# Kernel tuning notes

Hardware: AMD Instinct MI355X
Metric: run time of the kernel (lower is better)

## Reference

```python
import jax, jax.numpy as jnp
import numpy as np
import math

EMBED_DIM = 512
NUM_HEADS = 8
NUM_LAYERS = 6
NUM_CLASSES = 8
MAX_POS = 100
LN_EPS = 1e-5


def setup_inputs() -> dict:
    key = jax.random.key(0)
    ks = jax.random.split(key, 12)
    D, H, L, C = EMBED_DIM, NUM_HEADS, NUM_LAYERS, NUM_CLASSES
    B, M = 64, 20
    s = 0.02
    def p(k, shape):
        return jax.random.normal(k, shape, jnp.float32) * s
    return {
        "context_tokens": jax.random.normal(ks[0], (B, M, D), jnp.float32),
        "pos_enc": jax.random.normal(ks[1], (1, MAX_POS, D), jnp.float32),
        "sa_w": p(ks[2], (L, 3 * D, D)), "sa_b": jnp.zeros((L, 3 * D), jnp.float32),
        "sa_ow": p(ks[3], (L, D, D)), "sa_ob": jnp.zeros((L, D), jnp.float32),
        "ca_w": p(ks[4], (L, 3 * D, D)), "ca_b": jnp.zeros((L, 3 * D), jnp.float32),
        "ca_ow": p(ks[5], (L, D, D)), "ca_ob": jnp.zeros((L, D), jnp.float32),
        "ln1_g": jnp.ones((L, D), jnp.float32), "ln1_b": jnp.zeros((L, D), jnp.float32),
        "ln2_g": jnp.ones((L, D), jnp.float32), "ln2_b": jnp.zeros((L, D), jnp.float32),
        "ln3_g": jnp.ones((L, D), jnp.float32), "ln3_b": jnp.zeros((L, D), jnp.float32),
        "ffn_w1": p(ks[6], (L, 4 * D, D)), "ffn_b1": jnp.zeros((L, 4 * D), jnp.float32),
        "ffn_w2": p(ks[7], (L, D, 4 * D)), "ffn_b2": jnp.zeros((L, D), jnp.float32),
        "out_w": p(ks[8], (C, D)), "out_b": jnp.zeros((C,), jnp.float32),
        "max_tokens": 30,
    }


def _ln(x, g, b):
    m = jnp.mean(x, axis=-1, keepdims=True)
    v = jnp.mean(jnp.square(x - m), axis=-1, keepdims=True)
    return (x - m) * jax.lax.rsqrt(v + LN_EPS) * g + b


def _mha(q_in, kv_in, w, b, ow, ob, causal):
    # w: (3D, D) packed q/k/v projections (PyTorch in_proj), ow: (D, D)
    D = q_in.shape[-1]
    H = NUM_HEADS
    hd = D // H
    qw, kw, vw = w[:D], w[D:2 * D], w[2 * D:]
    bq, bk, bv = b[:D], b[D:2 * D], b[2 * D:]
    q = q_in @ qw.T + bq
    k = kv_in @ kw.T + bk
    v = kv_in @ vw.T + bv
    B, Sq = q.shape[0], q.shape[1]
    Sk = k.shape[1]
    q = q.reshape(B, Sq, H, hd)
    k = k.reshape(B, Sk, H, hd)
    v = v.reshape(B, Sk, H, hd)
    scores = jnp.einsum('bqhd,bkhd->bhqk', q, k) * (1.0 / math.sqrt(hd))
    if causal:
        mask = jnp.tril(jnp.ones((Sq, Sk), dtype=bool))
        scores = jnp.where(mask, scores, -jnp.inf)
    attn = jax.nn.softmax(scores, axis=-1)
    out = jnp.einsum('bhqk,bkhd->bqhd', attn, v).reshape(B, Sq, D)
    return out @ ow.T + ob


def _forward(context_tokens, pos_enc, sa_w, sa_b, sa_ow, sa_ob, ca_w, ca_b,
             ca_ow, ca_ob, ln1_g, ln1_b, ln2_g, ln2_b, ln3_g, ln3_b,
             ffn_w1, ffn_b1, ffn_w2, ffn_b2, out_w, out_b, max_tokens):
    gen = context_tokens  # (B, M, D), grows each step (full recompute, no KV cache)
    outs = []
    for t in range(max_tokens):
        S = gen.shape[1]
        x = gen + pos_enc[:, :S, :]
        for i in range(NUM_LAYERS):
            # norm_first pre-LN GPT-2 style TransformerDecoderLayer
            x = x + _mha(_ln(x, ln1_g[i], ln1_b[i]), _ln(x, ln1_g[i], ln1_b[i]),
                         sa_w[i], sa_b[i], sa_ow[i], sa_ob[i], causal=True)
            x = x + _mha(_ln(x, ln2_g[i], ln2_b[i]), context_tokens,
                         ca_w[i], ca_b[i], ca_ow[i], ca_ob[i], causal=False)
            h = _ln(x, ln3_g[i], ln3_b[i])
            h = jax.nn.gelu(h @ ffn_w1[i].T + ffn_b1[i], approximate=False)
            x = x + (h @ ffn_w2[i].T + ffn_b2[i])
        last = x[:, -1:, :]
        outs.append(last @ out_w.T + out_b)
        gen = jnp.concatenate([gen, last], axis=1)
    return jnp.concatenate(outs, axis=1)  # (B, max_tokens, num_classes)


def reference(context_tokens, pos_enc, sa_w, sa_b, sa_ow, sa_ob, ca_w, ca_b,
              ca_ow, ca_ob, ln1_g, ln1_b, ln2_g, ln2_b, ln3_g, ln3_b,
              ffn_w1, ffn_b1, ffn_w2, ffn_b2, out_w, out_b, max_tokens):
    return _forward(context_tokens, pos_enc, sa_w, sa_b, sa_ow, sa_ob, ca_w, ca_b,
                    ca_ow, ca_ob, ln1_g, ln1_b, ln2_g, ln2_b, ln3_g, ln3_b,
                    ffn_w1, ffn_b1, ffn_w2, ffn_b2, out_w, out_b, max_tokens)
```

## Files before the change

kernel.cpp:

```cpp
#include <hip/hip_runtime.h>
#include <math.h>

#define F4(p) (*reinterpret_cast<const float4*>(p))

constexpr int D    = 512;
constexpr int H    = 8;
constexpr int HD   = 64;
constexpr int NL   = 6;
constexpr int NB   = 64;
constexpr int M    = 20;
constexpr int T    = 30;
constexpr int SMAX = 49;
constexpr int NR   = NB * M;
constexpr float EPS   = 1e-5f;
constexpr float SCALE = 0.125f;

#define GM_PLAIN 0
#define GM_QKV   1

__device__ __forceinline__ float gelu_f(float x){
  return 0.5f * x * (1.f + erff(x * 0.70710678118654752f));
}

template<int K>
__device__ __forceinline__ float dot8(const float* __restrict__ w, const float* x, int j){
  float a0 = 0.f, a1 = 0.f;
  #pragma unroll
  for (int r = 0; r < K/64; r++){
    int d = j*4 + r*64;
    float4 w0 = F4(w + d);        float4 w1 = F4(w + d + 32);
    float4 x0 = F4(x + d);        float4 x1 = F4(x + d + 32);
    a0 += w0.x*x0.x + w0.y*x0.y + w0.z*x0.z + w0.w*x0.w;
    a1 += w1.x*x1.x + w1.y*x1.y + w1.z*x1.z + w1.w*x1.w;
  }
  float a = a0 + a1;
  a += __shfl_xor(a, 4, 8);
  a += __shfl_xor(a, 2, 8);
  a += __shfl_xor(a, 1, 8);
  return a;
}

__device__ __forceinline__ float dot16_2048(const float* __restrict__ w, const float* x, int j){
  float a0 = 0.f, a1 = 0.f;
  #pragma unroll
  for (int r = 0; r < 16; r++){
    int d = j*4 + r*128;
    float4 w0 = F4(w + d);        float4 w1 = F4(w + d + 64);
    float4 x0 = F4(x + d);        float4 x1 = F4(x + d + 64);
    a0 += w0.x*x0.x + w0.y*x0.y + w0.z*x0.z + w0.w*x0.w;
    a1 += w1.x*x1.x + w1.y*x1.y + w1.z*x1.z + w1.w*x1.w;
  }
  float a = a0 + a1;
  a += __shfl_xor(a, 8, 16);
  a += __shfl_xor(a, 4, 16);
  a += __shfl_xor(a, 2, 16);
  a += __shfl_xor(a, 1, 16);
  return a;
}


__device__ __forceinline__ float wave_sum64(float v){
  #pragma unroll
  for (int o = 32; o > 0; o >>= 1) v += __shfl_down(v, o, 64);
  return v;
}

__device__ __forceinline__ float block_sum256(float v, float* red){
  v = wave_sum64(v);
  int wid = threadIdx.x >> 6, lane = threadIdx.x & 63;
  if (lane == 0) red[wid] = v;
  __syncthreads();
  if (threadIdx.x == 0) red[0] = red[0] + red[1] + red[2] + red[3];
  __syncthreads();
  float tot = red[0];
  __syncthreads();
  return tot;
}

__global__ __launch_bounds__(256) void k_embed(const float* __restrict__ ctx,
    const float* __restrict__ pos, float* __restrict__ X0){
  int r = blockIdx.x, t = threadIdx.x, s = r % M;
  X0[(size_t)r*D + t]       = ctx[(size_t)r*D + t]       + pos[(size_t)s*D + t];
  X0[(size_t)r*D + t + 256] = ctx[(size_t)r*D + t + 256] + pos[(size_t)s*D + t + 256];
}

__global__ __launch_bounds__(256) void k_ln(const float* __restrict__ x, float* __restrict__ y,
    const float* __restrict__ g, const float* __restrict__ bb){
  __shared__ float red[4];
  int r = blockIdx.x, t = threadIdx.x;
  const float* xr = x + (size_t)r*D;
  float v0 = xr[t], v1 = xr[t+256];
  float mean = block_sum256(v0+v1, red) * (1.f/D);
  float d0 = v0-mean, d1 = v1-mean;
  float var = block_sum256(d0*d0 + d1*d1, red) * (1.f/D);
  float rs = rsqrtf(var + EPS);
  float* yr = y + (size_t)r*D;
  yr[t]     = d0*rs*g[t]     + bb[t];
  yr[t+256] = d1*rs*g[t+256] + bb[t+256];
}

__global__ __launch_bounds__(256) void k_gemm(
    const float* __restrict__ A, const float* __restrict__ W,
    const float* __restrict__ bias, const float* __restrict__ res,
    float* __restrict__ C, int K, int ldc, int gelu_flag,
    float* __restrict__ q0, float* __restrict__ kc, float* __restrict__ vc, int mode){
  __shared__ __align__(16) float As[32][64];
  __shared__ __align__(16) float Ws[32][64];
  int m0 = blockIdx.x*64, n0 = blockIdx.y*64;
  int t = threadIdx.x, tx = t & 15, ty = t >> 4;
  float acc[4][4] = {};
  for (int k0 = 0; k0 < K; k0 += 32){
    #pragma unroll
    for (int i = 0; i < 2; i++){
      int idx = t + i*256;
      int m = idx & 63, k4 = idx >> 6;
      float4 a = F4(A + (size_t)(m0+m)*K + k0 + k4*4);
      As[k4*4+0][m]=a.x; As[k4*4+1][m]=a.y; As[k4*4+2][m]=a.z; As[k4*4+3][m]=a.w;
      float4 w = F4(W + (size_t)(n0+m)*K + k0 + k4*4);
      Ws[k4*4+0][m]=w.x; Ws[k4*4+1][m]=w.y; Ws[k4*4+2][m]=w.z; Ws[k4*4+3][m]=w.w;
    }
    __syncthreads();
    #pragma unroll
    for (int k = 0; k < 32; k++){
      float4 a = *reinterpret_cast<float4*>(&As[k][ty*4]);
      float4 w = *reinterpret_cast<float4*>(&Ws[k][tx*4]);
      float av[4] = {a.x,a.y,a.z,a.w};
      float wv[4] = {w.x,w.y,w.z,w.w};
      #pragma unroll
      for (int i = 0; i < 4; i++)
        #pragma unroll
        for (int jj = 0; jj < 4; jj++) acc[i][jj] += av[i]*wv[jj];
    }
    __syncthreads();
  }
  #pragma unroll
  for (int i = 0; i < 4; i++){
    int row = m0 + ty*4 + i;
    #pragma unroll
    for (int jj = 0; jj < 4; jj++){
      int col = n0 + tx*4 + jj;
      float v = acc[i][jj] + bias[col];
      if (res) v += res[(size_t)row*ldc + col];
      if (gelu_flag) v = gelu_f(v);
      if (mode == GM_PLAIN){
        C[(size_t)row*ldc + col] = v;
      } else {
        if (col < D) q0[(size_t)row*D + col] = v;
        else {
          int b = row / M, s = row % M;
          float* dst = (col < 2*D) ? kc : vc;
          dst[((size_t)b*SMAX + s)*D + (col & (D-1))] = v;
        }
      }
    }
  }
}

__global__ __launch_bounds__(256) void k_sattn_pre(const float* __restrict__ Q0,
    const float* __restrict__ kc, const float* __restrict__ vc, float* __restrict__ AT0){
  int b = blockIdx.x >> 3, h = blockIdx.x & 7, t = threadIdx.x;
  __shared__ __align__(16) float q[M][HD], kk[M][HD], vv[M][HD];
  __shared__ float sc[M][M];
  for (int idx = t; idx < M*HD; idx += 256){
    int s = idx >> 6, e = idx & 63;
    q[s][e]  = Q0[((size_t)b*M + s)*D + h*HD + e];
    kk[s][e] = kc[((size_t)b*SMAX + s)*D + h*HD + e];
    vv[s][e] = vc[((size_t)b*SMAX + s)*D + h*HD + e];
  }
  __syncthreads();
  for (int idx = t; idx < M*M; idx += 256){
    int qs = idx / M, ks = idx % M;
    if (ks <= qs){
      float s = 0.f;
      #pragma unroll
      for (int e = 0; e < HD; e++) s += q[qs][e]*kk[ks][e];
      sc[qs][ks] = s * SCALE;
    }
  }
  __syncthreads();
  if (t < M){
    float mx = -1e30f;
    for (int ks = 0; ks <= t; ks++) mx = fmaxf(mx, sc[t][ks]);
    float sum = 0.f;
    for (int ks = 0; ks <= t; ks++){ float e = expf(sc[t][ks]-mx); sc[t][ks] = e; sum += e; }
    float inv = 1.f/sum;
    for (int ks = 0; ks <= t; ks++) sc[t][ks] *= inv;
  }
  __syncthreads();
  for (int idx = t; idx < M*HD; idx += 256){
    int qs = idx >> 6, e = idx & 63;
    float o = 0.f;
    for (int ks = 0; ks <= qs; ks++) o += sc[qs][ks]*vv[ks][e];
    AT0[((size_t)b*M + qs)*D + h*HD + e] = o;
  }
}

__global__ __launch_bounds__(256) void k_cattn_pre(const float* __restrict__ Q0,
    const float* __restrict__ ckv, float* __restrict__ AT0){
  int b = blockIdx.x >> 3, h = blockIdx.x & 7, t = threadIdx.x;
  __shared__ __align__(16) float q[M][HD], kk[M][HD], vv[M][HD];
  __shared__ float sc[M][M];
  for (int idx = t; idx < M*HD; idx += 256){
    int s = idx >> 6, e = idx & 63;
    q[s][e]  = Q0[((size_t)b*M + s)*D + h*HD + e];
    kk[s][e] = ckv[((size_t)b*M + s)*1024 + h*HD + e];
    vv[s][e] = ckv[((size_t)b*M + s)*1024 + D + h*HD + e];
  }
  __syncthreads();
  for (int idx = t; idx < M*M; idx += 256){
    int qs = idx / M, ks = idx % M;
    float s = 0.f;
    #pragma unroll
    for (int e = 0; e < HD; e++) s += q[qs][e]*kk[ks][e];
    sc[qs][ks] = s * SCALE;
  }
  __syncthreads();
  if (t < M){
    float mx = -1e30f;
    for (int ks = 0; ks < M; ks++) mx = fmaxf(mx, sc[t][ks]);
    float sum = 0.f;
    for (int ks = 0; ks < M; ks++){ float e = expf(sc[t][ks]-mx); sc[t][ks] = e; sum += e; }
    float inv = 1.f/sum;
    for (int ks = 0; ks < M; ks++) sc[t][ks] *= inv;
  }
  __syncthreads();
  for (int idx = t; idx < M*HD; idx += 256){
    int qs = idx >> 6, e = idx & 63;
    float o = 0.f;
    for (int ks = 0; ks < M; ks++) o += sc[qs][ks]*vv[ks][e];
    AT0[((size_t)b*M + qs)*D + h*HD + e] = o;
  }
}


__device__ __forceinline__ float bsum1024(float v, float* red, int t){
  #pragma unroll
  for (int o = 32; o > 0; o >>= 1) v += __shfl_xor(v, o, 64);
  if ((t & 63) == 0) red[t >> 6] = v;
  __syncthreads();
  if (t == 0){
    float s = 0.f;
    #pragma unroll
    for (int i = 0; i < 16; i++) s += red[i];
    red[16] = s;
  }
  __syncthreads();
  return red[16];
}

__device__ __forceinline__ void ln_ip(const float* xx, float* yy,
    const float* __restrict__ g, const float* __restrict__ bb, float* red, int t){
  float v = (t < D) ? xx[t] : 0.f;
  float mean = bsum1024(v, red, t) * (1.f/D);
  float dd = (t < D) ? (v - mean) : 0.f;
  float var = bsum1024(dd*dd, red, t) * (1.f/D);
  float rs = rsqrtf(var + EPS);
  if (t < D) yy[t] = dd*rs*g[t] + bb[t];
}

__device__ __forceinline__ void logits_pos(float* x, const float* __restrict__ outw,
    const float* __restrict__ outb, const float* __restrict__ pos,
    float* __restrict__ out, int b, int t, int st, int pn){
  if (t < D){
    int c = t >> 6, lane = t & 63;
    const float* wr = outw + (size_t)c*D + lane*8;
    const float* xr = x + lane*8;
    float4 w0 = F4(wr), w1 = F4(wr + 4);
    float4 x0 = F4(xr), x1 = F4(xr + 4);
    float a = w0.x*x0.x + w0.y*x0.y + w0.z*x0.z + w0.w*x0.w
            + w1.x*x1.x + w1.y*x1.y + w1.z*x1.z + w1.w*x1.w;
    #pragma unroll
    for (int o = 32; o > 0; o >>= 1) a += __shfl_xor(a, o, 64);
    if (lane == 0) out[((size_t)b*T + st)*8 + c] = a + outb[c];
  }
  __syncthreads();
  if (t < D) x[t] += pos[(size_t)pn*D + t];
  __syncthreads();
}

__global__ __launch_bounds__(1024) void k_chain(
    const float* __restrict__ X0, const float* __restrict__ pos,
    const float* __restrict__ sa_w, const float* __restrict__ sa_b,
    const float* __restrict__ sa_ow, const float* __restrict__ sa_ob,
    const float* __restrict__ ca_w, const float* __restrict__ ca_b,
    const float* __restrict__ ca_ow, const float* __restrict__ ca_ob,
    const float* __restrict__ ln1g, const float* __restrict__ ln1b,
    const float* __restrict__ ln2g, const float* __restrict__ ln2b,
    const float* __restrict__ ln3g, const float* __restrict__ ln3b,
    const float* __restrict__ fw1, const float* __restrict__ fb1,
    const float* __restrict__ fw2, const float* __restrict__ fb2,
    const float* __restrict__ outw, const float* __restrict__ outb,
    float* __restrict__ kcache, float* __restrict__ vcache,
    const float* __restrict__ ckv, float* __restrict__ out)
{
  const int b = blockIdx.x, t = threadIdx.x;
  const int j8 = t & 7, j16 = t & 15;
  __shared__ __align__(16) float x[D], xn[D], q[D], at[D], kcur[D], vcur[D];
  __shared__ __align__(16) float hh[2048];
  __shared__ float sc[H][SMAX + 7];
  __shared__ float red[17];

  if (t < D) x[t] = X0[((size_t)b*M + (M-1))*D + t];
  __syncthreads();

  logits_pos(x, outw, outb, pos, out, b, t, 0, M);

  for (int st = 1; st < T; st++){
    const int p = M - 1 + st, S = p + 1;
    for (int l = 0; l < NL; l++){
      float* kb = kcache + ((size_t)l*NB + b)*SMAX*D;
      float* vb = vcache + ((size_t)l*NB + b)*SMAX*D;
      const float* cb_ = ckv + ((size_t)l*NB + b)*M*1024;

      ln_ip(x, xn, ln1g + l*D, ln1b + l*D, red, t);
      __syncthreads();

      {
        const float* w = sa_w + (size_t)l*3*D*D;
        const float* bias = sa_b + (size_t)l*3*D;
        for (int pass = 0; pass < 12; pass++){
          int o = pass*128 + (t >> 3);
          float r = dot8<512>(w + (size_t)o*D, xn, j8);
          if (j8 == 0){
            r += bias[o];
            if (o < D) q[o] = r;
            else if (o < 2*D){ kcur[o-D] = r; kb[(size_t)p*D + (o-D)] = r; }
            else { vcur[o-2*D] = r; vb[(size_t)p*D + (o-2*D)] = r; }
          }
        }
      }
      __syncthreads();

      {
        int h = t >> 7, kslot = (t & 127) >> 3;
        const float* qh = q + h*HD;
        float4 x0 = F4(qh + j8*4), x1 = F4(qh + j8*4 + 32);
        for (int ks = kslot; ks < S; ks += 16){
          const float* kr = (ks == p) ? (kcur + h*HD) : (kb + (size_t)ks*D + h*HD);
          float4 w0 = F4(kr + j8*4), w1 = F4(kr + j8*4 + 32);
          float a = w0.x*x0.x + w0.y*x0.y + w0.z*x0.z + w0.w*x0.w
                  + w1.x*x1.x + w1.y*x1.y + w1.z*x1.z + w1.w*x1.w;
          a += __shfl_xor(a, 4, 8); a += __shfl_xor(a, 2, 8); a += __shfl_xor(a, 1, 8);
          if (j8 == 0) sc[h][ks] = a * SCALE;
        }
      }
      __syncthreads();
      if ((t >> 6) < H){
        int h = t >> 6, lane = t & 63;
        float v = (lane < S) ? sc[h][lane] : -1e30f;
        float mx = v;
        #pragma unroll
        for (int o = 32; o > 0; o >>= 1) mx = fmaxf(mx, __shfl_xor(mx, o, 64));
        float e = (lane < S) ? expf(v - mx) : 0.f;
        float sum = e;
        #pragma unroll
        for (int o = 32; o > 0; o >>= 1) sum += __shfl_xor(sum, o, 64);
        if (lane < S) sc[h][lane] = e / sum;
      }
      __syncthreads();
      if (t < D){
        int h = t >> 6, e = t & 63;
        float o2 = 0.f;
        for (int ks = 0; ks < p; ks++) o2 += sc[h][ks] * vb[(size_t)ks*D + h*HD + e];
        o2 += sc[h][p] * vcur[h*HD + e];
        at[t] = o2;
      }
      __syncthreads();

      {
        const float* w = sa_ow + (size_t)l*D*D;
        const float* bias = sa_ob + (size_t)l*D;
        for (int pass = 0; pass < 4; pass++){
          int o = pass*128 + (t >> 3);
          float r = dot8<512>(w + (size_t)o*D, at, j8);
          if (j8 == 0) x[o] += r + bias[o];
        }
      }
      __syncthreads();

      ln_ip(x, xn, ln2g + l*D, ln2b + l*D, red, t);
      __syncthreads();

      {
        const float* w = ca_w + (size_t)l*3*D*D;
        const float* bias = ca_b + (size_t)l*3*D;
        for (int pass = 0; pass < 4; pass++){
          int o = pass*128 + (t >> 3);
          float r = dot8<512>(w + (size_t)o*D, xn, j8);
          if (j8 == 0) q[o] = r + bias[o];
        }
      }
      __syncthreads();

      {
        int h = t >> 7, kslot = (t & 127) >> 3;
        const float* qh = q + h*HD;
        float4 x0 = F4(qh + j8*4), x1 = F4(qh + j8*4 + 32);
        for (int ks = kslot; ks < M; ks += 16){
          const float* kr = cb_ + (size_t)ks*1024 + h*HD;
          float4 w0 = F4(kr + j8*4), w1 = F4(kr + j8*4 + 32);
          float a = w0.x*x0.x + w0.y*x0.y + w0.z*x0.z + w0.w*x0.w
                  + w1.x*x1.x + w1.y*x1.y + w1.z*x1.z + w1.w*x1.w;
          a += __shfl_xor(a, 4, 8); a += __shfl_xor(a, 2, 8); a += __shfl_xor(a, 1, 8);
          if (j8 == 0) sc[h][ks] = a * SCALE;
        }
      }
      __syncthreads();
      if ((t >> 6) < H){
        int h = t >> 6, lane = t & 63;
        float v = (lane < M) ? sc[h][lane] : -1e30f;
        float mx = v;
        #pragma unroll
        for (int o = 32; o > 0; o >>= 1) mx = fmaxf(mx, __shfl_xor(mx, o, 64));
        float e = (lane < M) ? expf(v - mx) : 0.f;
        float sum = e;
        #pragma unroll
        for (int o = 32; o > 0; o >>= 1) sum += __shfl_xor(sum, o, 64);
        if (lane < M) sc[h][lane] = e / sum;
      }
      __syncthreads();
      if (t < D){
        int h = t >> 6, e = t & 63;
        float o2 = 0.f;
        for (int ks = 0; ks < M; ks++) o2 += sc[h][ks] * cb_[(size_t)ks*1024 + D + h*HD + e];
        at[t] = o2;
      }
      __syncthreads();

      {
        const float* w = ca_ow + (size_t)l*D*D;
        const float* bias = ca_ob + (size_t)l*D;
        for (int pass = 0; pass < 4; pass++){
          int o = pass*128 + (t >> 3);
          float r = dot8<512>(w + (size_t)o*D, at, j8);
          if (j8 == 0) x[o] += r + bias[o];
        }
      }
      __syncthreads();

      ln_ip(x, xn, ln3g + l*D, ln3b + l*D, red, t);
      __syncthreads();

      {
        const float* w = fw1 + (size_t)l*2048*D;
        const float* bias = fb1 + (size_t)l*2048;
        for (int pass = 0; pass < 16; pass++){
          int o = pass*128 + (t >> 3);
          float r = dot8<512>(w + (size_t)o*D, xn, j8);
          if (j8 == 0) hh[o] = gelu_f(r + bias[o]);
        }
      }
      __syncthreads();

      {
        const float* w = fw2 + (size_t)l*D*2048;
        const float* bias = fb2 + (size_t)l*D;
        for (int pass = 0; pass < 8; pass++){
          int o = pass*64 + (t >> 4);
          float r = dot16_2048(w + (size_t)o*2048, hh, j16);
          if (j16 == 0) x[o] += r + bias[o];
        }
      }
      __syncthreads();
    }
    logits_pos(x, outw, outb, pos, out, b, t, st, M + st);
  }
}


extern "C" void kernel_launch(void* const* d_in, const int* in_sizes, int n_in,
                              void* d_out, int out_size, void* d_ws, size_t ws_size,
                              hipStream_t stream){
  (void)in_sizes; (void)n_in; (void)out_size; (void)ws_size;
  const float* ctx   = (const float*)d_in[0];
  const float* pos   = (const float*)d_in[1];
  const float* sa_w  = (const float*)d_in[2];
  const float* sa_b  = (const float*)d_in[3];
  const float* sa_ow = (const float*)d_in[4];
  const float* sa_ob = (const float*)d_in[5];
  const float* ca_w  = (const float*)d_in[6];
  const float* ca_b  = (const float*)d_in[7];
  const float* ca_ow = (const float*)d_in[8];
  const float* ca_ob = (const float*)d_in[9];
  const float* ln1g  = (const float*)d_in[10];
  const float* ln1b  = (const float*)d_in[11];
  const float* ln2g  = (const float*)d_in[12];
  const float* ln2b  = (const float*)d_in[13];
  const float* ln3g  = (const float*)d_in[14];
  const float* ln3b  = (const float*)d_in[15];
  const float* fw1   = (const float*)d_in[16];
  const float* fb1   = (const float*)d_in[17];
  const float* fw2   = (const float*)d_in[18];
  const float* fb2   = (const float*)d_in[19];
  const float* outw  = (const float*)d_in[20];
  const float* outb  = (const float*)d_in[21];
  float* out = (float*)d_out;

  float* w = (float*)d_ws;
  size_t off = 0;
  auto alloc = [&](size_t n){ float* p = w + off; off += n; return p; };
  float* kcache = alloc((size_t)NL*NB*SMAX*D);
  float* vcache = alloc((size_t)NL*NB*SMAX*D);
  float* ckv    = alloc((size_t)NL*NB*M*1024);
  float* X0     = alloc((size_t)NR*D);
  float* XN0    = alloc((size_t)NR*D);
  float* Q0     = alloc((size_t)NR*D);
  float* AT0    = alloc((size_t)NR*D);
  float* H0     = alloc((size_t)NR*2048);

  dim3 blk(256);

  k_embed<<<NR, blk, 0, stream>>>(ctx, pos, X0);
  for (int l = 0; l < NL; l++){
    k_gemm<<<dim3(NR/64, 1024/64), blk, 0, stream>>>(
        ctx, ca_w + (size_t)l*3*D*D + (size_t)D*D, ca_b + (size_t)l*3*D + D, nullptr,
        ckv + (size_t)l*NB*M*1024, 512, 1024, 0, nullptr, nullptr, nullptr, GM_PLAIN);
  }

  for (int l = 0; l < NL; l++){
    const float* saw = sa_w + (size_t)l*3*D*D;
    const float* sab = sa_b + (size_t)l*3*D;
    float* kcl = kcache + (size_t)l*NB*SMAX*D;
    float* vcl = vcache + (size_t)l*NB*SMAX*D;
    const float* ckl = ckv + (size_t)l*NB*M*1024;

    k_ln<<<NR, blk, 0, stream>>>(X0, XN0, ln1g + l*D, ln1b + l*D);
    k_gemm<<<dim3(NR/64, 1536/64), blk, 0, stream>>>(
        XN0, saw, sab, nullptr, nullptr, 512, D, 0, Q0, kcl, vcl, GM_QKV);
    k_sattn_pre<<<NB*H, blk, 0, stream>>>(Q0, kcl, vcl, AT0);
    k_gemm<<<dim3(NR/64, D/64), blk, 0, stream>>>(
        AT0, sa_ow + (size_t)l*D*D, sa_ob + l*D, X0, X0, 512, D, 0,
        nullptr, nullptr, nullptr, GM_PLAIN);
    k_ln<<<NR, blk, 0, stream>>>(X0, XN0, ln2g + l*D, ln2b + l*D);
    k_gemm<<<dim3(NR/64, D/64), blk, 0, stream>>>(
        XN0, ca_w + (size_t)l*3*D*D, ca_b + (size_t)l*3*D, nullptr, Q0, 512, D, 0,
        nullptr, nullptr, nullptr, GM_PLAIN);
    k_cattn_pre<<<NB*H, blk, 0, stream>>>(Q0, ckl, AT0);
    k_gemm<<<dim3(NR/64, D/64), blk, 0, stream>>>(
        AT0, ca_ow + (size_t)l*D*D, ca_ob + l*D, X0, X0, 512, D, 0,
        nullptr, nullptr, nullptr, GM_PLAIN);
    k_ln<<<NR, blk, 0, stream>>>(X0, XN0, ln3g + l*D, ln3b + l*D);
    k_gemm<<<dim3(NR/64, 2048/64), blk, 0, stream>>>(
        XN0, fw1 + (size_t)l*2048*D, fb1 + (size_t)l*2048, nullptr, H0, 512, 2048, 1,
        nullptr, nullptr, nullptr, GM_PLAIN);
    k_gemm<<<dim3(NR/64, D/64), blk, 0, stream>>>(
        H0, fw2 + (size_t)l*D*2048, fb2 + l*D, X0, X0, 2048, D, 0,
        nullptr, nullptr, nullptr, GM_PLAIN);
  }

  k_chain<<<NB, dim3(1024), 0, stream>>>(
      X0, pos, sa_w, sa_b, sa_ow, sa_ob, ca_w, ca_b, ca_ow, ca_ob,
      ln1g, ln1b, ln2g, ln2b, ln3g, ln3b, fw1, fb1, fw2, fb2,
      outw, outb, kcache, vcache, ckv, out);
}
```

Baseline: 42.30 ms.

## Split decode weight columns across blocks with grid-wide barriers

Replaces the per-batch decode kernel, where each of 64 blocks streamed the full weight matrices for its one sequence, with a persistent kernel in which each block owns a slice of output columns for all 64 batch rows. Blocks are synchronised by a software grid barrier built on atomics between phases. Each weight row is now read once per step and reused across the batch rows, instead of being re-read by all 64 blocks. LayerNorm is fused into the projection phases. The cost is about ten grid barriers per layer per step, and activations must round-trip through global memory between phases.

```diff
diff --git a/kernel.cpp b/kernel.cpp
--- a/kernel.cpp
+++ b/kernel.cpp
@@ -12,6 +12,7 @@
 constexpr int T    = 30;
 constexpr int SMAX = 49;
 constexpr int NR   = NB * M;
+constexpr int NBLK = 64;
 constexpr float EPS   = 1e-5f;
 constexpr float SCALE = 0.125f;
 
@@ -20,42 +21,6 @@
 
 __device__ __forceinline__ float gelu_f(float x){
   return 0.5f * x * (1.f + erff(x * 0.70710678118654752f));
-}
-
-template<int K>
-__device__ __forceinline__ float dot8(const float* __restrict__ w, const float* x, int j){
-  float a0 = 0.f, a1 = 0.f;
-  #pragma unroll
-  for (int r = 0; r < K/64; r++){
-    int d = j*4 + r*64;
-    float4 w0 = F4(w + d);        float4 w1 = F4(w + d + 32);
-    float4 x0 = F4(x + d);        float4 x1 = F4(x + d + 32);
-    a0 += w0.x*x0.x + w0.y*x0.y + w0.z*x0.z + w0.w*x0.w;
-    a1 += w1.x*x1.x + w1.y*x1.y + w1.z*x1.z + w1.w*x1.w;
-  }
-  float a = a0 + a1;
-  a += __shfl_xor(a, 4, 8);
-  a += __shfl_xor(a, 2, 8);
-  a += __shfl_xor(a, 1, 8);
-  return a;
-}
-
-__device__ __forceinline__ float dot16_2048(const float* __restrict__ w, const float* x, int j){
-  float a0 = 0.f, a1 = 0.f;
-  #pragma unroll
-  for (int r = 0; r < 16; r++){
-    int d = j*4 + r*128;
-    float4 w0 = F4(w + d);        float4 w1 = F4(w + d + 64);
-    float4 x0 = F4(x + d);        float4 x1 = F4(x + d + 64);
-    a0 += w0.x*x0.x + w0.y*x0.y + w0.z*x0.z + w0.w*x0.w;
-    a1 += w1.x*x1.x + w1.y*x1.y + w1.z*x1.z + w1.w*x1.w;
-  }
-  float a = a0 + a1;
-  a += __shfl_xor(a, 8, 16);
-  a += __shfl_xor(a, 4, 16);
-  a += __shfl_xor(a, 2, 16);
-  a += __shfl_xor(a, 1, 16);
-  return a;
 }
 
 
@@ -233,52 +198,198 @@
 }
 
 
-__device__ __forceinline__ float bsum1024(float v, float* red, int t){
-  #pragma unroll
-  for (int o = 32; o > 0; o >>= 1) v += __shfl_xor(v, o, 64);
-  if ((t & 63) == 0) red[t >> 6] = v;
-  __syncthreads();
-  if (t == 0){
-    float s = 0.f;
-    #pragma unroll
-    for (int i = 0; i < 16; i++) s += red[i];
-    red[16] = s;
-  }
-  __syncthreads();
-  return red[16];
-}
-
-__device__ __forceinline__ void ln_ip(const float* xx, float* yy,
-    const float* __restrict__ g, const float* __restrict__ bb, float* red, int t){
-  float v = (t < D) ? xx[t] : 0.f;
-  float mean = bsum1024(v, red, t) * (1.f/D);
-  float dd = (t < D) ? (v - mean) : 0.f;
-  float var = bsum1024(dd*dd, red, t) * (1.f/D);
-  float rs = rsqrtf(var + EPS);
-  if (t < D) yy[t] = dd*rs*g[t] + bb[t];
-}
-
-__device__ __forceinline__ void logits_pos(float* x, const float* __restrict__ outw,
-    const float* __restrict__ outb, const float* __restrict__ pos,
-    float* __restrict__ out, int b, int t, int st, int pn){
-  if (t < D){
-    int c = t >> 6, lane = t & 63;
-    const float* wr = outw + (size_t)c*D + lane*8;
-    const float* xr = x + lane*8;
-    float4 w0 = F4(wr), w1 = F4(wr + 4);
+__device__ __forceinline__ void gsync(unsigned* cnt, unsigned* gen, unsigned target){
+  __syncthreads();
+  if (threadIdx.x == 0){
+    __threadfence();
+    unsigned a = __hip_atomic_fetch_add(cnt, 1u, __ATOMIC_ACQ_REL, __HIP_MEMORY_SCOPE_AGENT);
+    if (a == NBLK - 1){
+      __hip_atomic_store(cnt, 0u, __ATOMIC_RELAXED, __HIP_MEMORY_SCOPE_AGENT);
+      __hip_atomic_store(gen, target, __ATOMIC_RELEASE, __HIP_MEMORY_SCOPE_AGENT);
+    } else {
+      while (__hip_atomic_load(gen, __ATOMIC_ACQUIRE, __HIP_MEMORY_SCOPE_AGENT) < target)
+        __builtin_amdgcn_s_sleep(2);
+    }
+    __threadfence();
+  }
+  __syncthreads();
+}
+
+template<int C, int MODE, bool LN, bool GELU>
+__device__ __forceinline__ void col_phase(
+    const float* __restrict__ src,
+    const float* __restrict__ wb, const float* __restrict__ bias,
+    const float* __restrict__ g, const float* __restrict__ bb,
+    float* __restrict__ dst, int ldc,
+    float* __restrict__ qdst, float* __restrict__ kbp, float* __restrict__ vbp,
+    float* __restrict__ X, int bk, int t)
+{
+  __shared__ __align__(16) float xs[16][520];
+  const int j8 = t & 7, o0 = bk * C;
+  #pragma unroll 1
+  for (int tile = 0; tile < 4; tile++){
+    {
+      int r = t >> 6, lane = t & 63;
+      int rg = tile*16 + r;
+      const float* sr = src + (size_t)rg*D + lane*8;
+      float4 a = F4(sr), b4 = F4(sr + 4);
+      float mval = 0.f, rsv = 1.f;
+      if constexpr (LN){
+        float s  = a.x+a.y+a.z+a.w + b4.x+b4.y+b4.z+b4.w;
+        float s2 = a.x*a.x+a.y*a.y+a.z*a.z+a.w*a.w
+                 + b4.x*b4.x+b4.y*b4.y+b4.z*b4.z+b4.w*b4.w;
+        #pragma unroll
+        for (int o = 32; o > 0; o >>= 1){ s += __shfl_xor(s,o,64); s2 += __shfl_xor(s2,o,64); }
+        mval = s * (1.f/512.f);
+        float var = s2 * (1.f/512.f) - mval*mval;
+        rsv = rsqrtf(var + EPS);
+      }
+      float* xr = &xs[r][lane*8];
+      if constexpr (LN){
+        const float* gp = g + lane*8; const float* bp = bb + lane*8;
+        float4 g0 = F4(gp), g1 = F4(gp+4), c0 = F4(bp), c1 = F4(bp+4);
+        float4 o0v, o1v;
+        o0v.x=(a.x -mval)*rsv*g0.x+c0.x; o0v.y=(a.y -mval)*rsv*g0.y+c0.y;
+        o0v.z=(a.z -mval)*rsv*g0.z+c0.z; o0v.w=(a.w -mval)*rsv*g0.w+c0.w;
+        o1v.x=(b4.x-mval)*rsv*g1.x+c1.x; o1v.y=(b4.y-mval)*rsv*g1.y+c1.y;
+        o1v.z=(b4.z-mval)*rsv*g1.z+c1.z; o1v.w=(b4.w-mval)*rsv*g1.w+c1.w;
+        *reinterpret_cast<float4*>(xr)   = o0v;
+        *reinterpret_cast<float4*>(xr+4) = o1v;
+      } else {
+        *reinterpret_cast<float4*>(xr)   = a;
+        *reinterpret_cast<float4*>(xr+4) = b4;
+      }
+    }
+    __syncthreads();
+    constexpr int NOUT = 16*C;
+    constexpr int PER  = NOUT / 128;
+    #pragma unroll
+    for (int i = 0; i < PER; i++){
+      int oi = (t >> 3) + i*128;
+      int c = oi >> 4, r = oi & 15;
+      const float* w = wb + (size_t)(o0 + c)*D;
+      const float* xr = xs[r];
+      float a0 = 0.f, a1 = 0.f;
+      #pragma unroll
+      for (int u = 0; u < 8; u++){
+        int d = j8*4 + u*64;
+        float4 w0 = F4(w + d), w1 = F4(w + d + 32);
+        float4 x0 = F4(xr + d), x1 = F4(xr + d + 32);
+        a0 += w0.x*x0.x + w0.y*x0.y + w0.z*x0.z + w0.w*x0.w;
+        a1 += w1.x*x1.x + w1.y*x1.y + w1.z*x1.z + w1.w*x1.w;
+      }
+      float a = a0 + a1;
+      a += __shfl_xor(a,4,8); a += __shfl_xor(a,2,8); a += __shfl_xor(a,1,8);
+      if (j8 == 0){
+        int o = o0 + c, rg = tile*16 + r;
+        float v = a + bias[o];
+        if constexpr (GELU) v = gelu_f(v);
+        if constexpr (MODE == 0){
+          dst[(size_t)rg*ldc + o] = v;
+        } else if constexpr (MODE == 1){
+          if (o < D)            qdst[(size_t)rg*D + o] = v;
+          else if (o < 2*D)     kbp[(size_t)rg*SMAX*D + (o - D)] = v;
+          else                  vbp[(size_t)rg*SMAX*D + (o - 2*D)] = v;
+        } else {
+          X[(size_t)rg*D + o] += v;
+        }
+      }
+    }
+    __syncthreads();
+  }
+}
+
+__device__ __forceinline__ void ffn2_phase(const float* __restrict__ HH,
+    const float* __restrict__ wb, const float* __restrict__ bias,
+    float* __restrict__ X, int bk, int t){
+  int gp = t >> 3, j8 = t & 7;
+  int r = gp >> 1, ch = gp & 1;
+  const float* hrow = HH + (size_t)r*2048;
+  #pragma unroll 1
+  for (int ci = 0; ci < 4; ci++){
+    int o = bk*8 + ch*4 + ci;
+    const float* w = wb + (size_t)o*2048;
+    float a0 = 0.f, a1 = 0.f;
+    #pragma unroll 8
+    for (int u = 0; u < 32; u++){
+      int d = j8*4 + u*64;
+      float4 w0 = F4(w + d), w1 = F4(w + d + 32);
+      float4 x0 = F4(hrow + d), x1 = F4(hrow + d + 32);
+      a0 += w0.x*x0.x + w0.y*x0.y + w0.z*x0.z + w0.w*x0.w;
+      a1 += w1.x*x1.x + w1.y*x1.y + w1.z*x1.z + w1.w*x1.w;
+    }
+    float a = a0 + a1;
+    a += __shfl_xor(a,4,8); a += __shfl_xor(a,2,8); a += __shfl_xor(a,1,8);
+    if (j8 == 0) X[(size_t)r*D + o] += a + bias[o];
+  }
+}
+
+__device__ __forceinline__ void attn_phase(const float* __restrict__ Q,
+    const float* __restrict__ kb, const float* __restrict__ vb, size_t kstride,
+    float* __restrict__ AT, int S, int bk, int t){
+  __shared__ float sc[8*56];
+  __shared__ float avp[1024];
+  int gp = t >> 3, j8 = t & 7;
+  {
+    int h = gp >> 4, kslot = gp & 15;
+    const float* qh = Q + (size_t)bk*D + h*HD + j8*4;
+    float4 q0 = F4(qh), q1 = F4(qh + 32);
+    for (int ks = kslot; ks < S; ks += 16){
+      const float* kr = kb + (size_t)ks*kstride + h*HD + j8*4;
+      float4 w0 = F4(kr), w1 = F4(kr + 32);
+      float a = w0.x*q0.x + w0.y*q0.y + w0.z*q0.z + w0.w*q0.w
+              + w1.x*q1.x + w1.y*q1.y + w1.z*q1.z + w1.w*q1.w;
+      a += __shfl_xor(a,4,8); a += __shfl_xor(a,2,8); a += __shfl_xor(a,1,8);
+      if (j8 == 0) sc[h*56 + ks] = a * SCALE;
+    }
+  }
+  __syncthreads();
+  if (t < 512){
+    int h2 = t >> 6, lane = t & 63;
+    float v = (lane < S) ? sc[h2*56 + lane] : -1e30f;
+    float mx = v;
+    #pragma unroll
+    for (int o = 32; o > 0; o >>= 1) mx = fmaxf(mx, __shfl_xor(mx,o,64));
+    float e = (lane < S) ? expf(v - mx) : 0.f;
+    float sum = e;
+    #pragma unroll
+    for (int o = 32; o > 0; o >>= 1) sum += __shfl_xor(sum,o,64);
+    if (lane < S) sc[h2*56 + lane] = e / sum;
+  }
+  __syncthreads();
+  {
+    int tt = t & 511, half = t >> 9;
+    int h2 = tt >> 6, e = tt & 63;
+    const float* vcol = vb + h2*HD + e;
+    float o2 = 0.f;
+    for (int ks = half; ks < S; ks += 2) o2 += sc[h2*56 + ks] * vcol[(size_t)ks*kstride];
+    avp[half*512 + tt] = o2;
+  }
+  __syncthreads();
+  if (t < 512) AT[(size_t)bk*D + t] = avp[t] + avp[512 + t];
+}
+
+__device__ __forceinline__ void finalize_phase(float* __restrict__ X,
+    const float* __restrict__ outw, const float* __restrict__ outb,
+    const float* __restrict__ pos, float* __restrict__ out,
+    int st, int pn, int bk, int t){
+  int w = t >> 6, lane = t & 63;
+  if (w < 8){
+    const float* ww = outw + (size_t)w*D + lane*8;
+    const float* xr = X + (size_t)bk*D + lane*8;
+    float4 w0 = F4(ww), w1 = F4(ww + 4);
     float4 x0 = F4(xr), x1 = F4(xr + 4);
     float a = w0.x*x0.x + w0.y*x0.y + w0.z*x0.z + w0.w*x0.w
             + w1.x*x1.x + w1.y*x1.y + w1.z*x1.z + w1.w*x1.w;
     #pragma unroll
-    for (int o = 32; o > 0; o >>= 1) a += __shfl_xor(a, o, 64);
-    if (lane == 0) out[((size_t)b*T + st)*8 + c] = a + outb[c];
-  }
-  __syncthreads();
-  if (t < D) x[t] += pos[(size_t)pn*D + t];
-  __syncthreads();
-}
-
-__global__ __launch_bounds__(1024) void k_chain(
+    for (int o = 32; o > 0; o >>= 1) a += __shfl_xor(a,o,64);
+    if (lane == 0) out[((size_t)bk*T + st)*8 + w] = a + outb[w];
+  }
+  __syncthreads();
+  if (t < D) X[(size_t)bk*D + t] += pos[(size_t)pn*D + t];
+}
+
+__global__ __launch_bounds__(1024, 1) void k_decode(
     const float* __restrict__ X0, const float* __restrict__ pos,
     const float* __restrict__ sa_w, const float* __restrict__ sa_b,
     const float* __restrict__ sa_ow, const float* __restrict__ sa_ob,
@@ -291,179 +402,51 @@
     const float* __restrict__ fw2, const float* __restrict__ fb2,
     const float* __restrict__ outw, const float* __restrict__ outb,
     float* __restrict__ kcache, float* __restrict__ vcache,
-    const float* __restrict__ ckv, float* __restrict__ out)
+    const float* __restrict__ ckv, float* __restrict__ X,
+    float* __restrict__ Q, float* __restrict__ AT, float* __restrict__ HH,
+    unsigned* cnt, unsigned* gen, float* __restrict__ out)
 {
-  const int b = blockIdx.x, t = threadIdx.x;
-  const int j8 = t & 7, j16 = t & 15;
-  __shared__ __align__(16) float x[D], xn[D], q[D], at[D], kcur[D], vcur[D];
-  __shared__ __align__(16) float hh[2048];
-  __shared__ float sc[H][SMAX + 7];
-  __shared__ float red[17];
-
-  if (t < D) x[t] = X0[((size_t)b*M + (M-1))*D + t];
-  __syncthreads();
-
-  logits_pos(x, outw, outb, pos, out, b, t, 0, M);
+  const int bk = blockIdx.x, t = threadIdx.x;
+  unsigned tgt = 0;
+
+  if (t < D) X[(size_t)bk*D + t] = X0[((size_t)bk*M + (M-1))*D + t];
+  gsync(cnt, gen, ++tgt);
+  finalize_phase(X, outw, outb, pos, out, 0, M, bk, t);
+  gsync(cnt, gen, ++tgt);
 
   for (int st = 1; st < T; st++){
     const int p = M - 1 + st, S = p + 1;
     for (int l = 0; l < NL; l++){
-      float* kb = kcache + ((size_t)l*NB + b)*SMAX*D;
-      float* vb = vcache + ((size_t)l*NB + b)*SMAX*D;
-      const float* cb_ = ckv + ((size_t)l*NB + b)*M*1024;
-
-      ln_ip(x, xn, ln1g + l*D, ln1b + l*D, red, t);
-      __syncthreads();
-
+      float* kbp = kcache + (size_t)l*NB*SMAX*D + (size_t)p*D;
+      float* vbp = vcache + (size_t)l*NB*SMAX*D + (size_t)p*D;
+      col_phase<24,1,true,false>(X, sa_w + (size_t)l*3*D*D, sa_b + l*3*D,
+          ln1g + l*D, ln1b + l*D, nullptr, 0, Q, kbp, vbp, nullptr, bk, t);
+      gsync(cnt, gen, ++tgt);
+      attn_phase(Q, kcache + ((size_t)l*NB + bk)*SMAX*D,
+                    vcache + ((size_t)l*NB + bk)*SMAX*D, D, AT, S, bk, t);
+      gsync(cnt, gen, ++tgt);
+      col_phase<8,2,false,false>(AT, sa_ow + (size_t)l*D*D, sa_ob + l*D,
+          nullptr, nullptr, nullptr, 0, nullptr, nullptr, nullptr, X, bk, t);
+      gsync(cnt, gen, ++tgt);
+      col_phase<8,0,true,false>(X, ca_w + (size_t)l*3*D*D, ca_b + l*3*D,
+          ln2g + l*D, ln2b + l*D, Q, D, nullptr, nullptr, nullptr, nullptr, bk, t);
+      gsync(cnt, gen, ++tgt);
       {
-        const float* w = sa_w + (size_t)l*3*D*D;
-        const float* bias = sa_b + (size_t)l*3*D;
-        for (int pass = 0; pass < 12; pass++){
-          int o = pass*128 + (t >> 3);
-          float r = dot8<512>(w + (size_t)o*D, xn, j8);
-          if (j8 == 0){
-            r += bias[o];
-            if (o < D) q[o] = r;
-            else if (o < 2*D){ kcur[o-D] = r; kb[(size_t)p*D + (o-D)] = r; }
-            else { vcur[o-2*D] = r; vb[(size_t)p*D + (o-2*D)] = r; }
-          }
-        }
+        const float* cb_ = ckv + ((size_t)l*NB + bk)*M*1024;
+        attn_phase(Q, cb_, cb_ + D, 1024, AT, M, bk, t);
       }
-      __syncthreads();
-
-      {
-        int h = t >> 7, kslot = (t & 127) >> 3;
-        const float* qh = q + h*HD;
-        float4 x0 = F4(qh + j8*4), x1 = F4(qh + j8*4 + 32);
-        for (int ks = kslot; ks < S; ks += 16){
-          const float* kr = (ks == p) ? (kcur + h*HD) : (kb + (size_t)ks*D + h*HD);
-          float4 w0 = F4(kr + j8*4), w1 = F4(kr + j8*4 + 32);
-          float a = w0.x*x0.x + w0.y*x0.y + w0.z*x0.z + w0.w*x0.w
-                  + w1.x*x1.x + w1.y*x1.y + w1.z*x1.z + w1.w*x1.w;
-          a += __shfl_xor(a, 4, 8); a += __shfl_xor(a, 2, 8); a += __shfl_xor(a, 1, 8);
-          if (j8 == 0) sc[h][ks] = a * SCALE;
-        }
-      }
-      __syncthreads();
-      if ((t >> 6) < H){
-        int h = t >> 6, lane = t & 63;
-        float v = (lane < S) ? sc[h][lane] : -1e30f;
-        float mx = v;
-        #pragma unroll
-        for (int o = 32; o > 0; o >>= 1) mx = fmaxf(mx, __shfl_xor(mx, o, 64));
-        float e = (lane < S) ? expf(v - mx) : 0.f;
-        float sum = e;
-        #pragma unroll
-        for (int o = 32; o > 0; o >>= 1) sum += __shfl_xor(sum, o, 64);
-        if (lane < S) sc[h][lane] = e / sum;
-      }
-      __syncthreads();
-      if (t < D){
-        int h = t >> 6, e = t & 63;
-        float o2 = 0.f;
-        for (int ks = 0; ks < p; ks++) o2 += sc[h][ks] * vb[(size_t)ks*D + h*HD + e];
-        o2 += sc[h][p] * vcur[h*HD + e];
-        at[t] = o2;
-      }
-      __syncthreads();
-
-      {
-        const float* w = sa_ow + (size_t)l*D*D;
-        const float* bias = sa_ob + (size_t)l*D;
-        for (int pass = 0; pass < 4; pass++){
-          int o = pass*128 + (t >> 3);
-          float r = dot8<512>(w + (size_t)o*D, at, j8);
-          if (j8 == 0) x[o] += r + bias[o];
-        }
-      }
-      __syncthreads();
-
-      ln_ip(x, xn, ln2g + l*D, ln2b + l*D, red, t);
-      __syncthreads();
-
-      {
-        const float* w = ca_w + (size_t)l*3*D*D;
-        const float* bias = ca_b + (size_t)l*3*D;
-        for (int pass = 0; pass < 4; pass++){
-          int o = pass*128 + (t >> 3);
-          float r = dot8<512>(w + (size_t)o*D, xn, j8);
-          if (j8 == 0) q[o] = r + bias[o];
-        }
-      }
-      __syncthreads();
-
-      {
-        int h = t >> 7, kslot = (t & 127) >> 3;
-        const float* qh = q + h*HD;
-        float4 x0 = F4(qh + j8*4), x1 = F4(qh + j8*4 + 32);
-        for (int ks = kslot; ks < M; ks += 16){
-          const float* kr = cb_ + (size_t)ks*1024 + h*HD;
-          float4 w0 = F4(kr + j8*4), w1 = F4(kr + j8*4 + 32);
-          float a = w0.x*x0.x + w0.y*x0.y + w0.z*x0.z + w0.w*x0.w
-                  + w1.x*x1.x + w1.y*x1.y + w1.z*x1.z + w1.w*x1.w;
-          a += __shfl_xor(a, 4, 8); a += __shfl_xor(a, 2, 8); a += __shfl_xor(a, 1, 8);
-          if (j8 == 0) sc[h][ks] = a * SCALE;
-        }
-      }
-      __syncthreads();
-      if ((t >> 6) < H){
-        int h = t >> 6, lane = t & 63;
-        float v = (lane < M) ? sc[h][lane] : -1e30f;
-        float mx = v;
-        #pragma unroll
-        for (int o = 32; o > 0; o >>= 1) mx = fmaxf(mx, __shfl_xor(mx, o, 64));
-        float e = (lane < M) ? expf(v - mx) : 0.f;
-        float sum = e;
-        #pragma unroll
-        for (int o = 32; o > 0; o >>= 1) sum += __shfl_xor(sum, o, 64);
-        if (lane < M) sc[h][lane] = e / sum;
-      }
-      __syncthreads();
-      if (t < D){
-        int h = t >> 6, e = t & 63;
-        float o2 = 0.f;
-        for (int ks = 0; ks < M; ks++) o2 += sc[h][ks] * cb_[(size_t)ks*1024 + D + h*HD + e];
-        at[t] = o2;
-      }
-      __syncthreads();
-
-      {
-        const float* w = ca_ow + (size_t)l*D*D;
-        const float* bias = ca_ob + (size_t)l*D;
-        for (int pass = 0; pass < 4; pass++){
-          int o = pass*128 + (t >> 3);
-          float r = dot8<512>(w + (size_t)o*D, at, j8);
-          if (j8 == 0) x[o] += r + bias[o];
-        }
-      }
-      __syncthreads();
-
-      ln_ip(x, xn, ln3g + l*D, ln3b + l*D, red, t);
-      __syncthreads();
-
-      {
-        const float* w = fw1 + (size_t)l*2048*D;
-        const float* bias = fb1 + (size_t)l*2048;
-        for (int pass = 0; pass < 16; pass++){
-          int o = pass*128 + (t >> 3);
-          float r = dot8<512>(w + (size_t)o*D, xn, j8);
-          if (j8 == 0) hh[o] = gelu_f(r + bias[o]);
-        }
-      }
-      __syncthreads();
-
-      {
-        const float* w = fw2 + (size_t)l*D*2048;
-        const float* bias = fb2 + (size_t)l*D;
-        for (int pass = 0; pass < 8; pass++){
-          int o = pass*64 + (t >> 4);
-          float r = dot16_2048(w + (size_t)o*2048, hh, j16);
-          if (j16 == 0) x[o] += r + bias[o];
-        }
-      }
-      __syncthreads();
-    }
-    logits_pos(x, outw, outb, pos, out, b, t, st, M + st);
+      gsync(cnt, gen, ++tgt);
+      col_phase<8,2,false,false>(AT, ca_ow + (size_t)l*D*D, ca_ob + l*D,
+          nullptr, nullptr, nullptr, 0, nullptr, nullptr, nullptr, X, bk, t);
+      gsync(cnt, gen, ++tgt);
+      col_phase<32,0,true,true>(X, fw1 + (size_t)l*2048*D, fb1 + l*2048,
+          ln3g + l*D, ln3b + l*D, HH, 2048, nullptr, nullptr, nullptr, nullptr, bk, t);
+      gsync(cnt, gen, ++tgt);
+      ffn2_phase(HH, fw2 + (size_t)l*D*2048, fb2 + l*D, X, bk, t);
+      gsync(cnt, gen, ++tgt);
+    }
+    finalize_phase(X, outw, outb, pos, out, st, M + st, bk, t);
+    gsync(cnt, gen, ++tgt);
   }
 }
 
@@ -507,6 +490,13 @@
   float* Q0     = alloc((size_t)NR*D);
   float* AT0    = alloc((size_t)NR*D);
   float* H0     = alloc((size_t)NR*2048);
+  float* Xd     = alloc((size_t)NB*D);
+  float* Qd     = alloc((size_t)NB*D);
+  float* ATd    = alloc((size_t)NB*D);
+  float* HHd    = alloc((size_t)NB*2048);
+  unsigned* bar = (unsigned*)(w + off); off += 256;
+
+  hipMemsetAsync(bar, 0, 1024, stream);
 
   dim3 blk(256);
 
@@ -548,8 +538,9 @@
         nullptr, nullptr, nullptr, GM_PLAIN);
   }
 
-  k_chain<<<NB, dim3(1024), 0, stream>>>(
+  k_decode<<<NBLK, dim3(1024), 0, stream>>>(
       X0, pos, sa_w, sa_b, sa_ow, sa_ob, ca_w, ca_b, ca_ow, ca_ob,
       ln1g, ln1b, ln2g, ln2b, ln3g, ln3b, fw1, fb1, fw2, fb2,
-      outw, outb, kcache, vcache, ckv, out);
-}
+      outw, outb, kcache, vcache, ckv, Xd, Qd, ATd, HHd,
+      bar, bar + 64, out);
+}
```

After: 87.29 ms. 106% more time.
